# Kernel optimization log

Hardware: AMD Instinct MI355X
Metric: run time of the kernel (lower is better)

## Reference

```python
import jax, jax.numpy as jnp
import numpy as np

EPS = 1e-6  # F.normalize eps

N, C, H, W = 2, 64, 64, 64
HEADS, DK, DV = 2, 64, 32


def setup_inputs() -> dict:
    key = jax.random.key(0)
    ks = jax.random.split(key, 9)
    w = lambda k, sh: jax.random.normal(k, sh, jnp.float32) * 0.05
    return {
        "x":  jax.random.normal(ks[0], (N, C, H, W), jnp.float32),
        "Wq": w(ks[1], (HEADS, DK, C)), "bq": w(ks[2], (HEADS, DK)),
        "Wk": w(ks[3], (HEADS, DK, C)), "bk": w(ks[4], (HEADS, DK)),
        "Wv": w(ks[5], (HEADS, DV, C)), "bv": w(ks[6], (HEADS, DV)),
        "Wm": w(ks[7], (C, HEADS * DV)), "bm": w(ks[8], (C,)),
    }


def _l2norm(t):
    # F.normalize(dim=1) on [N, dk, L]; here heads are stacked: [N, h, dk, L], axis=2
    n = jnp.linalg.norm(t, axis=2, keepdims=True)
    return t / jnp.maximum(n, EPS)


def reference(x, Wq, bq, Wk, bk, Wv, bv, Wm, bm):
    n, c, h, w = x.shape
    L = h * w
    xf = x.reshape(n, c, L)  # 1x1 conv == pointwise channel GEMM; x_enc = x (no pos enc)
    Q = jnp.einsum('hkc,ncl->nhkl', Wq, xf) + bq[None, :, :, None]
    K = jnp.einsum('hkc,ncl->nhkl', Wk, xf) + bk[None, :, :, None]
    V = jnp.einsum('hvc,ncl->nhvl', Wv, xf) + bv[None, :, :, None]
    Q = _l2norm(Q)
    K = _l2norm(K)
    # cosine-similarity attention: contract over dk, softmax over keys
    A = jax.nn.softmax(jnp.einsum('nhkl,nhkm->nhlm', Q, K), axis=-1)  # [n,h,L,L]
    R = jnp.einsum('nhlm,nhvm->nhvl', A, V)  # [n,h,dv,L]
    Rc = R.reshape(n, -1, L)  # concat heads along channels
    out = jnp.einsum('oc,ncl->nol', Wm, Rc) + bm[None, :, None]
    return out.reshape(n, c, h, w) + x  # residual
```

## Files before the change

kernel.cpp:

```cpp
#include <hip/hip_runtime.h>
#include <cmath>


typedef __bf16 bf16x8 __attribute__((ext_vector_type(8)));
typedef __bf16 bf16x4 __attribute__((ext_vector_type(4)));
typedef float f4_t __attribute__((ext_vector_type(4)));

#define LQ 4096
#define NH 4
#define KS 8

__device__ inline f4_t mfma16(bf16x8 a, bf16x8 b, f4_t c) {
    return __builtin_amdgcn_mfma_f32_16x16x32_bf16(a, b, c, 0, 0, 0);
}

__device__ inline bf16x8 cvt8(const float* p) {
    f4_t a = *(const f4_t*)p, b = *(const f4_t*)(p + 4);
    bf16x8 r;
    r[0] = (__bf16)a[0]; r[1] = (__bf16)a[1]; r[2] = (__bf16)a[2]; r[3] = (__bf16)a[3];
    r[4] = (__bf16)b[0]; r[5] = (__bf16)b[1]; r[6] = (__bf16)b[2]; r[7] = (__bf16)b[3];
    return r;
}

__device__ inline void gload_lds16(const __bf16* g, __bf16* l) {
    __builtin_amdgcn_global_load_lds(
        (const __attribute__((address_space(1))) void*)g,
        (__attribute__((address_space(3))) void*)l, 16, 0, 0);
}

__global__ __launch_bounds__(256) void k1_qkv(
        const float* __restrict__ x,
        const float* __restrict__ Wq, const float* __restrict__ bq,
        const float* __restrict__ Wk, const float* __restrict__ bk,
        const float* __restrict__ Wv, const float* __restrict__ bv,
        __bf16* __restrict__ Qb, __bf16* __restrict__ Kb,
        __bf16* __restrict__ Vtb) {
    const int tid  = threadIdx.x;
    const int lane = tid & 63;
    const int w    = tid >> 6;
    const int quad = lane >> 4;
    const int l15  = lane & 15;
    const int lt   = blockIdx.x;
    const int n    = blockIdx.y;
    const int l0   = lt * 32;

    __shared__ __bf16 xl[32][72];

    {
        const int c0 = tid >> 5, l = tid & 31;
#pragma unroll
        for (int i = 0; i < 8; ++i) {
            const int c = c0 + i * 8;
            xl[l][c] = (__bf16)x[((size_t)n * 64 + c) * LQ + l0 + l];
        }
    }

    const float* Wqk = (w < 2) ? Wq : Wk;
    const float* bqk = (w < 2) ? bq : bk;
    const int h = w & 1;

    bf16x8 af[4][2], av[2];
#pragma unroll
    for (int t = 0; t < 4; ++t)
#pragma unroll
        for (int kh = 0; kh < 2; ++kh)
            af[t][kh] = cvt8(Wqk + (size_t)(h * 64 + t * 16 + l15) * 64
                                  + kh * 32 + quad * 8);
#pragma unroll
    for (int kh = 0; kh < 2; ++kh)
        av[kh] = cvt8(Wv + (size_t)(w * 16 + l15) * 64 + kh * 32 + quad * 8);

    f4_t binit[4], bvinit;
#pragma unroll
    for (int t = 0; t < 4; ++t)
#pragma unroll
        for (int r = 0; r < 4; ++r)
            binit[t][r] = bqk[h * 64 + t * 16 + quad * 4 + r];
#pragma unroll
    for (int r = 0; r < 4; ++r)
        bvinit[r] = bv[w * 16 + quad * 4 + r];

    __syncthreads();

    f4_t acc[4][2], vacc[2];
#pragma unroll
    for (int lsub = 0; lsub < 2; ++lsub) {
        bf16x8 bf0 = *(const bf16x8*)&xl[lsub * 16 + l15][quad * 8];
        bf16x8 bf1 = *(const bf16x8*)&xl[lsub * 16 + l15][32 + quad * 8];
#pragma unroll
        for (int t = 0; t < 4; ++t) {
            f4_t a = mfma16(af[t][0], bf0, binit[t]);
            acc[t][lsub] = mfma16(af[t][1], bf1, a);
        }
        f4_t va = mfma16(av[0], bf0, bvinit);
        vacc[lsub] = mfma16(av[1], bf1, va);
    }

    const int nh = n * 2 + h;
    __bf16* dst  = (w < 2) ? Qb : Kb;
    const float post = (w < 2) ? 1.44269504f : 1.0f;
#pragma unroll
    for (int lsub = 0; lsub < 2; ++lsub) {
        float ss = 0.f;
#pragma unroll
        for (int t = 0; t < 4; ++t)
#pragma unroll
            for (int r = 0; r < 4; ++r)
                ss = fmaf(acc[t][lsub][r], acc[t][lsub][r], ss);
        ss += __shfl_xor(ss, 16, 64);
        ss += __shfl_xor(ss, 32, 64);
        const float rn = post / fmaxf(sqrtf(ss), 1e-6f);

        const int l = l0 + lsub * 16 + l15;
#pragma unroll
        for (int t = 0; t < 4; ++t) {
            bf16x4 pk;
#pragma unroll
            for (int r = 0; r < 4; ++r) pk[r] = (__bf16)(acc[t][lsub][r] * rn);
            const int kc = t * 2 + (quad >> 1);
            *(bf16x4*)(dst + ((size_t)(nh * 8 + kc) * LQ + l) * 8 + (quad & 1) * 4) = pk;
        }
#pragma unroll
        for (int r = 0; r < 4; ++r) {
            const int vrow = w * 16 + quad * 4 + r;
            Vtb[(size_t)(n * 64 + vrow) * LQ + l] = (__bf16)vacc[lsub][r];
        }
    }
}

__global__ __launch_bounds__(256, 4) void k2_attn(
        const __bf16* __restrict__ Qb, const __bf16* __restrict__ Kb,
        const __bf16* __restrict__ Vtb,
        __bf16* __restrict__ numPb, float* __restrict__ denP) {
    const int tid  = threadIdx.x;
    const int lane = tid & 63;
    const int wave = tid >> 6;
    const int quad = lane >> 4;
    const int l15  = lane & 15;
    const int nh   = blockIdx.y;
    const int ks   = blockIdx.z;
    const int qbase = blockIdx.x * 128 + wave * 32;
    const int kbase = ks * 512;

    __shared__ __bf16 Kl[2][4096];
    __shared__ __bf16 P[4][2][16][72];

    const f4_t fzero = {0.f, 0.f, 0.f, 0.f};

    const __bf16* s_src0, * s_src1;
    {
        const int s0 = tid, s1 = tid + 256;
        const int kc0 = ((s0 >> 6) & 1) * 4 + ((s0 >> 4) & 3);
        const int ll0 = (s0 >> 7) * 16 + (s0 & 15);
        const int kc1 = ((s1 >> 6) & 1) * 4 + ((s1 >> 4) & 3);
        const int ll1 = (s1 >> 7) * 16 + (s1 & 15);
        s_src0 = Kb + ((size_t)(nh * 8 + kc0) * LQ + kbase + ll0) * 8;
        s_src1 = Kb + ((size_t)(nh * 8 + kc1) * LQ + kbase + ll1) * 8;
    }

    bf16x8 qf[2][2];
#pragma unroll
    for (int qt = 0; qt < 2; ++qt)
#pragma unroll
        for (int kh = 0; kh < 2; ++kh)
            qf[qt][kh] = *(const bf16x8*)(Qb +
                ((size_t)(nh * 8 + kh * 4 + quad) * LQ + qbase + qt * 16 + l15) * 8);

    f4_t racc[2][2];
#pragma unroll
    for (int a = 0; a < 2; ++a)
#pragma unroll
        for (int b = 0; b < 2; ++b) racc[a][b] = fzero;
    float den[2] = {0.f, 0.f};

    const __bf16* v_src = Vtb + (size_t)(nh * 32 + l15) * LQ + kbase + quad * 8;

    gload_lds16(s_src0, &Kl[0][wave * 512]);
    gload_lds16(s_src1, &Kl[0][2048 + wave * 512]);
    __syncthreads();

#pragma unroll 2
    for (int ch = 0; ch < 8; ++ch) {
        const int cur = ch & 1;

        if (ch < 7) {
            gload_lds16(s_src0 + (size_t)(ch + 1) * 512,
                        &Kl[cur ^ 1][wave * 512]);
            gload_lds16(s_src1 + (size_t)(ch + 1) * 512,
                        &Kl[cur ^ 1][2048 + wave * 512]);
        }

        bf16x8 vf[2][2];
#pragma unroll
        for (int vt = 0; vt < 2; ++vt)
#pragma unroll
            for (int kp = 0; kp < 2; ++kp)
                vf[vt][kp] = *(const bf16x8*)(v_src + (size_t)vt * 16 * LQ
                                              + ch * 64 + kp * 32);

#pragma unroll
        for (int ktp = 0; ktp < 2; ++ktp) {
            bf16x8 kf[2][2];
#pragma unroll
            for (int i = 0; i < 2; ++i)
#pragma unroll
                for (int kh = 0; kh < 2; ++kh)
                    kf[i][kh] = *(const bf16x8*)
                        &Kl[cur][(size_t)((ktp * 2 + i) * 128 + kh * 64
                                          + quad * 16 + l15) * 8];

            f4_t s[2][2];
#pragma unroll
            for (int qt = 0; qt < 2; ++qt)
#pragma unroll
                for (int i = 0; i < 2; ++i) {
                    f4_t t = mfma16(kf[i][0], qf[qt][0], fzero);
                    s[qt][i] = mfma16(kf[i][1], qf[qt][1], t);
                }

#pragma unroll
            for (int qt = 0; qt < 2; ++qt)
#pragma unroll
                for (int i = 0; i < 2; ++i) {
                    bf16x4 pv;
                    float d = 0.f;
#pragma unroll
                    for (int r = 0; r < 4; ++r) {
                        float p = __builtin_exp2f(s[qt][i][r]);
                        d += p;
                        pv[r] = (__bf16)p;
                    }
                    den[qt] += d;
                    *(bf16x4*)&P[wave][qt][l15][(ktp * 2 + i) * 16 + quad * 4] = pv;
                }
        }

#pragma unroll
        for (int qt = 0; qt < 2; ++qt)
#pragma unroll
            for (int kp = 0; kp < 2; ++kp) {
                bf16x8 pf = *(const bf16x8*)&P[wave][qt][l15][kp * 32 + quad * 8];
                racc[0][qt] = mfma16(vf[0][kp], pf, racc[0][qt]);
                racc[1][qt] = mfma16(vf[1][kp], pf, racc[1][qt]);
            }

        __syncthreads();
    }

#pragma unroll
    for (int qt = 0; qt < 2; ++qt) {
        den[qt] += __shfl_xor(den[qt], 16, 64);
        den[qt] += __shfl_xor(den[qt], 32, 64);
    }

    const size_t pb = (size_t)(nh * KS + ks) * LQ;
#pragma unroll
    for (int vt = 0; vt < 2; ++vt)
#pragma unroll
        for (int qt = 0; qt < 2; ++qt) {
            bf16x4 pk;
#pragma unroll
            for (int r = 0; r < 4; ++r) pk[r] = (__bf16)racc[vt][qt][r];
            *(bf16x4*)(numPb + (pb + qbase + qt * 16 + l15) * 32
                             + vt * 16 + quad * 4) = pk;
        }

    if (lane < 16)
#pragma unroll
        for (int qt = 0; qt < 2; ++qt)
            denP[pb + qbase + qt * 16 + lane] = den[qt];
}

__global__ __launch_bounds__(256) void k3_out(
        const __bf16* __restrict__ numPb, const float* __restrict__ denP,
        const float* __restrict__ Wm, const float* __restrict__ bm,
        const float* __restrict__ x, float* __restrict__ out) {
    const int tid = threadIdx.x;
    const int lt  = blockIdx.x;
    const int n   = blockIdx.y;
    const int l0  = lt * 16;

    __shared__ float Rps[2][64][17];
    __shared__ float dinv[2][16];

    if (tid < 32) {
        const int hh = tid >> 4, li = tid & 15;
        float s = 0.f;
#pragma unroll
        for (int k = 0; k < KS; ++k)
            s += denP[(size_t)((n * 2 + hh) * KS + k) * LQ + l0 + li];
        dinv[hh][li] = 1.0f / s;
    }

    {
        const int vg = tid & 3, l = (tid >> 2) & 15;
        const int hh = (tid >> 6) & 1, sh = tid >> 7;
        const size_t base = (size_t)(n * 2 + hh) * KS * LQ;
        float a[8] = {0.f, 0.f, 0.f, 0.f, 0.f, 0.f, 0.f, 0.f};
#pragma unroll
        for (int k = 0; k < 4; ++k) {
            const int kk = sh * 4 + k;
            bf16x8 v8 = *(const bf16x8*)(numPb +
                (base + (size_t)kk * LQ + l0 + l) * 32 + vg * 8);
#pragma unroll
            for (int j = 0; j < 8; ++j) a[j] += (float)v8[j];
        }
#pragma unroll
        for (int j = 0; j < 8; ++j)
            Rps[sh][hh * 32 + vg * 8 + j][l] = a[j];
    }
    __syncthreads();

    const int l = tid & 15, og = tid >> 4;
    const float d0 = dinv[0][l], d1 = dinv[1][l];
    float rj[64];
#pragma unroll
    for (int j = 0; j < 64; ++j)
        rj[j] = (Rps[0][j][l] + Rps[1][j][l]) * (j < 32 ? d0 : d1);

#pragma unroll
    for (int oi = 0; oi < 4; ++oi) {
        const int o = og * 4 + oi;
        const float* wr = Wm + (size_t)o * 64;
        float a = bm[o];
#pragma unroll
        for (int j4 = 0; j4 < 16; ++j4) {
            f4_t t = *(const f4_t*)(wr + j4 * 4);
            a = fmaf(t[0], rj[j4 * 4 + 0], a);
            a = fmaf(t[1], rj[j4 * 4 + 1], a);
            a = fmaf(t[2], rj[j4 * 4 + 2], a);
            a = fmaf(t[3], rj[j4 * 4 + 3], a);
        }
        const size_t idx = (size_t)(n * 64 + o) * LQ + l0 + l;
        out[idx] = a + x[idx];
    }
}

extern "C" void kernel_launch(void* const* d_in, const int* in_sizes, int n_in,
                              void* d_out, int out_size, void* d_ws, size_t ws_size,
                              hipStream_t stream) {
    const float* x  = (const float*)d_in[0];
    const float* Wq = (const float*)d_in[1];
    const float* bq = (const float*)d_in[2];
    const float* Wk = (const float*)d_in[3];
    const float* bk = (const float*)d_in[4];
    const float* Wv = (const float*)d_in[5];
    const float* bv = (const float*)d_in[6];
    const float* Wm = (const float*)d_in[7];
    const float* bm = (const float*)d_in[8];
    float* out = (float*)d_out;

    __bf16* Qb    = (__bf16*)d_ws;
    __bf16* Kb    = Qb + (size_t)NH * LQ * 64;
    __bf16* Vtb   = Kb + (size_t)NH * LQ * 64;
    __bf16* numPb = Vtb + (size_t)NH * 32 * LQ;
    float*  denP  = (float*)(numPb + (size_t)NH * KS * LQ * 32);

    k1_qkv<<<dim3(128, 2), dim3(256), 0, stream>>>(x, Wq, bq, Wk, bk, Wv, bv,
                                                   Qb, Kb, Vtb);
    k2_attn<<<dim3(32, NH, KS), dim3(256), 0, stream>>>(Qb, Kb, Vtb, numPb, denP);
    k3_out<<<dim3(256, 2), dim3(256), 0, stream>>>(numPb, denP, Wm, bm, x, out);
}
```

Measured before the change: 112.2 us.

## Keep softmax probabilities in registers via permuted K layout; double key splits

The K tile is now loaded into LDS with a permuted key ordering. As a result, the S=K·Q MFMA output registers line up with the B-operand layout of the P·V MFMA. This removes the per-wave P shared-memory staging buffer, its writes and reads, and lets V fragments be loaded per sub-tile. Key splits double from 8 to 16, with half as many chunks per block, and launch bounds now request 8 blocks per CU. The aim is more parallelism and occupancy, at the cost of twice as many partial sums to reduce in the final kernel.

```diff
diff --git a/kernel.cpp b/kernel.cpp
--- a/kernel.cpp
+++ b/kernel.cpp
@@ -8,7 +8,8 @@
 
 #define LQ 4096
 #define NH 4
-#define KS 8
+#define KS 16
+#define CH 4
 
 __device__ inline f4_t mfma16(bf16x8 a, bf16x8 b, f4_t c) {
     return __builtin_amdgcn_mfma_f32_16x16x32_bf16(a, b, c, 0, 0, 0);
@@ -128,7 +129,7 @@
     }
 }
 
-__global__ __launch_bounds__(256, 4) void k2_attn(
+__global__ __launch_bounds__(256, 8) void k2_attn(
         const __bf16* __restrict__ Qb, const __bf16* __restrict__ Kb,
         const __bf16* __restrict__ Vtb,
         __bf16* __restrict__ numPb, float* __restrict__ denP) {
@@ -140,10 +141,9 @@
     const int nh   = blockIdx.y;
     const int ks   = blockIdx.z;
     const int qbase = blockIdx.x * 128 + wave * 32;
-    const int kbase = ks * 512;
+    const int kbase = ks * 256;
 
     __shared__ __bf16 Kl[2][4096];
-    __shared__ __bf16 P[4][2][16][72];
 
     const f4_t fzero = {0.f, 0.f, 0.f, 0.f};
 
@@ -151,9 +151,11 @@
     {
         const int s0 = tid, s1 = tid + 256;
         const int kc0 = ((s0 >> 6) & 1) * 4 + ((s0 >> 4) & 3);
-        const int ll0 = (s0 >> 7) * 16 + (s0 & 15);
+        const int ll0 = ((s0 >> 8) << 5) + (((s0 >> 2) & 3) << 3)
+                      + (((s0 >> 7) & 1) << 2) + (s0 & 3);
         const int kc1 = ((s1 >> 6) & 1) * 4 + ((s1 >> 4) & 3);
-        const int ll1 = (s1 >> 7) * 16 + (s1 & 15);
+        const int ll1 = ((s1 >> 8) << 5) + (((s1 >> 2) & 3) << 3)
+                      + (((s1 >> 7) & 1) << 2) + (s1 & 3);
         s_src0 = Kb + ((size_t)(nh * 8 + kc0) * LQ + kbase + ll0) * 8;
         s_src1 = Kb + ((size_t)(nh * 8 + kc1) * LQ + kbase + ll1) * 8;
     }
@@ -180,26 +182,24 @@
     __syncthreads();
 
 #pragma unroll 2
-    for (int ch = 0; ch < 8; ++ch) {
+    for (int ch = 0; ch < CH; ++ch) {
         const int cur = ch & 1;
 
-        if (ch < 7) {
+        if (ch < CH - 1) {
             gload_lds16(s_src0 + (size_t)(ch + 1) * 512,
                         &Kl[cur ^ 1][wave * 512]);
             gload_lds16(s_src1 + (size_t)(ch + 1) * 512,
                         &Kl[cur ^ 1][2048 + wave * 512]);
         }
 
-        bf16x8 vf[2][2];
-#pragma unroll
-        for (int vt = 0; vt < 2; ++vt)
-#pragma unroll
-            for (int kp = 0; kp < 2; ++kp)
-                vf[vt][kp] = *(const bf16x8*)(v_src + (size_t)vt * 16 * LQ
-                                              + ch * 64 + kp * 32);
-
 #pragma unroll
         for (int ktp = 0; ktp < 2; ++ktp) {
+            bf16x8 vf[2];
+#pragma unroll
+            for (int vt = 0; vt < 2; ++vt)
+                vf[vt] = *(const bf16x8*)(v_src + (size_t)vt * 16 * LQ
+                                          + ch * 64 + ktp * 32);
+
             bf16x8 kf[2][2];
 #pragma unroll
             for (int i = 0; i < 2; ++i)
@@ -219,30 +219,22 @@
                 }
 
 #pragma unroll
-            for (int qt = 0; qt < 2; ++qt)
-#pragma unroll
-                for (int i = 0; i < 2; ++i) {
-                    bf16x4 pv;
-                    float d = 0.f;
+            for (int qt = 0; qt < 2; ++qt) {
+                bf16x8 pf;
+                float d = 0.f;
+#pragma unroll
+                for (int i = 0; i < 2; ++i)
 #pragma unroll
                     for (int r = 0; r < 4; ++r) {
                         float p = __builtin_exp2f(s[qt][i][r]);
                         d += p;
-                        pv[r] = (__bf16)p;
+                        pf[i * 4 + r] = (__bf16)p;
                     }
-                    den[qt] += d;
-                    *(bf16x4*)&P[wave][qt][l15][(ktp * 2 + i) * 16 + quad * 4] = pv;
-                }
-        }
-
-#pragma unroll
-        for (int qt = 0; qt < 2; ++qt)
-#pragma unroll
-            for (int kp = 0; kp < 2; ++kp) {
-                bf16x8 pf = *(const bf16x8*)&P[wave][qt][l15][kp * 32 + quad * 8];
-                racc[0][qt] = mfma16(vf[0][kp], pf, racc[0][qt]);
-                racc[1][qt] = mfma16(vf[1][kp], pf, racc[1][qt]);
+                den[qt] += d;
+                racc[0][qt] = mfma16(vf[0], pf, racc[0][qt]);
+                racc[1][qt] = mfma16(vf[1], pf, racc[1][qt]);
             }
+        }
 
         __syncthreads();
     }
@@ -298,8 +290,8 @@
         const size_t base = (size_t)(n * 2 + hh) * KS * LQ;
         float a[8] = {0.f, 0.f, 0.f, 0.f, 0.f, 0.f, 0.f, 0.f};
 #pragma unroll
-        for (int k = 0; k < 4; ++k) {
-            const int kk = sh * 4 + k;
+        for (int k = 0; k < 8; ++k) {
+            const int kk = sh * 8 + k;
             bf16x8 v8 = *(const bf16x8*)(numPb +
                 (base + (size_t)kk * LQ + l0 + l) * 32 + vg * 8);
 #pragma unroll
```

Measured after the change: 248.4 us. 121% more time.
